# Optimization experiments

Measured on AMD Instinct MI355X. Metric: run time of the kernel, lower is better.

## Reference

```python
import jax, jax.numpy as jnp
import numpy as np

B, T, M, Q = 1024, 336, 1, 9
DFF, H, L = 7, 1024, 2
D_IN = DFF + M      # decoder input per step
D_OUT = M * Q       # quantile outputs per step


def setup_inputs() -> dict:
    key = jax.random.key(0)
    ks = jax.random.split(key, 16)
    s = 1.0 / np.sqrt(H)

    def rn(k, shape, scale):
        return (jax.random.normal(k, shape, jnp.float32) * scale).astype(jnp.float32)

    return {
        "batchsize": B,
        "Y_teacher": rn(ks[0], (B, T, M), 1.0),
        "inp_y": rn(ks[1], (B, 1, M), 1.0),
        "h": rn(ks[2], (L, B, H), 0.1),
        "c": rn(ks[3], (L, B, H), 0.1),
        "future_features": rn(ks[4], (B, T, DFF), 1.0),
        "horizon_span": T,
        "teacher_forcing": 0,
        "teacher_forcing_prob": 0,
        # LSTM layer 0 (input size D_IN) and layer 1 (input size H), PyTorch i,f,g,o gate order
        "W_ih0": rn(ks[5], (4 * H, D_IN), s),
        "W_hh0": rn(ks[6], (4 * H, H), s),
        "b_ih0": rn(ks[7], (4 * H,), s),
        "b_hh0": rn(ks[8], (4 * H,), s),
        "W_ih1": rn(ks[9], (4 * H, H), s),
        "W_hh1": rn(ks[10], (4 * H, H), s),
        "b_ih1": rn(ks[11], (4 * H,), s),
        "b_hh1": rn(ks[12], (4 * H,), s),
        # output projection d_hidden -> M*Q
        "W_out": rn(ks[13], (D_OUT, H), s),
        "b_out": rn(ks[14], (D_OUT,), s),
    }


def reference(batchsize, Y_teacher, inp_y, h, c, future_features, horizon_span,
              teacher_forcing, teacher_forcing_prob,
              W_ih0, W_hh0, b_ih0, b_hh0, W_ih1, W_hh1, b_ih1, b_hh1,
              W_out, b_out):
    m = inp_y.shape[-1]
    Wih = (W_ih0, W_ih1)
    Whh = (W_hh0, W_hh1)
    bih = (b_ih0, b_ih1)
    bhh = (b_hh0, b_hh1)

    def step(carry, f_t):
        hs, cs, y_prev = carry            # hs,cs: [L,B,H]; y_prev: [B,M]; f_t: [B,DFF]
        x = jnp.concatenate([y_prev, f_t], axis=-1)   # [B, D_IN]
        new_h, new_c = [], []
        for l in range(len(Wih)):
            gates = x @ Wih[l].T + bih[l] + hs[l] @ Whh[l].T + bhh[l]  # [B, 4H]
            i_, f_, g_, o_ = jnp.split(gates, 4, axis=-1)
            c_new = jax.nn.sigmoid(f_) * cs[l] + jax.nn.sigmoid(i_) * jnp.tanh(g_)
            h_new = jax.nn.sigmoid(o_) * jnp.tanh(c_new)
            new_h.append(h_new)
            new_c.append(c_new)
            x = h_new
        y = x @ W_out.T + b_out           # [B, M*Q]
        return (jnp.stack(new_h), jnp.stack(new_c), y[:, :m]), y

    ff = jnp.swapaxes(future_features, 0, 1)          # [T, B, DFF]
    _, ys = jax.lax.scan(step, (h, c, inp_y[:, 0, :]), ff)
    out = jnp.swapaxes(ys, 0, 1)                      # [B, T, M*Q]
    return out.reshape(batchsize, horizon_span, m, -1)
```

## Files before the change

### kernel.cpp

```cpp
#include <hip/hip_runtime.h>

typedef _Float16 f16;
typedef __attribute__((ext_vector_type(8))) _Float16 f16x8;
typedef __attribute__((ext_vector_type(4))) float f32x4;

#define NBATCH 1024
#define NH 1024
#define NT 336
#define NDFF 7
#define NQ 9
#define K0 1088
#define K1 2048
#define OUTSTRIDE (NT * NQ)

__device__ __forceinline__ float sigf(float x) { return 1.0f / (1.0f + __expf(-x)); }
__device__ __forceinline__ float tanhfast(float x) { return 1.0f - 2.0f / (__expf(2.0f * x) + 1.0f); }

__device__ __forceinline__ void gll16(const void* g, void* l) {
  __builtin_amdgcn_global_load_lds((const __attribute__((address_space(1))) void*)g,
                                   (__attribute__((address_space(3))) void*)l, 16, 0, 0);
}

__global__ void pack_w0(const float* __restrict__ Wih0, const float* __restrict__ Whh0,
                        f16* __restrict__ Wp0) {
  const int idx = blockIdx.x * 256 + threadIdx.x;
  if (idx >= 4096 * K0) return;
  const int j = idx / K0;
  const int dk = idx - j * K0;
  const int sk = (dk & ~63) | ((dk & 63) ^ ((j & 7) << 3));
  float v;
  if (sk < 8) v = Wih0[j * 8 + sk];
  else if (sk < 64) v = 0.0f;
  else v = Whh0[(size_t)j * NH + (sk - 64)];
  Wp0[idx] = (f16)v;
}

__global__ void pack_w1(const float* __restrict__ Wih1, const float* __restrict__ Whh1,
                        f16* __restrict__ Wp1) {
  const int idx = blockIdx.x * 256 + threadIdx.x;
  const int j = idx >> 11;
  const int dk = idx & 2047;
  const int sk = (dk & ~63) | ((dk & 63) ^ ((j & 7) << 3));
  const float v = (sk < 1024) ? Wih1[(size_t)j * NH + sk]
                              : Whh1[(size_t)j * NH + (sk - 1024)];
  Wp1[idx] = (f16)v;
}

__global__ void pack_bias(const float* __restrict__ a0, const float* __restrict__ b0,
                          const float* __restrict__ a1, const float* __restrict__ b1,
                          float* __restrict__ bias0, float* __restrict__ bias1) {
  const int j = blockIdx.x * 256 + threadIdx.x;
  if (j < 4096) { bias0[j] = a0[j] + b0[j]; bias1[j] = a1[j] + b1[j]; }
}

__global__ void init_state(const float* __restrict__ h_in, const float* __restrict__ c_in,
                           f16* __restrict__ h0, f16* __restrict__ h1,
                           float* __restrict__ c0, float* __restrict__ c1) {
  const int idx = blockIdx.x * 256 + threadIdx.x;
  const int l = idx >> 20;
  const int rc = idx & 1048575;
  const int row = rc >> 10;
  const int dk = idx & 1023;
  const int sk = (dk & ~63) | ((dk & 63) ^ ((row & 7) << 3));
  const float hv = h_in[((size_t)l << 20) + ((size_t)row << 10) + sk];
  if (l == 0) { h0[rc] = (f16)hv; c0[rc] = c_in[idx]; }
  else        { h1[rc] = (f16)hv; c1[rc] = c_in[idx]; }
}

__global__ void final_y(const float* __restrict__ ypartT, const float* __restrict__ bout,
                        float* __restrict__ dout) {
  const int idx = blockIdx.x * 256 + threadIdx.x;
  const int row = idx & 1023;
  const int q = idx >> 10;
  float s = bout[q];
#pragma unroll
  for (int nb2 = 0; nb2 < 32; ++nb2) s += ypartT[(((q << 5) + nb2) << 10) + row];
  dout[(size_t)row * OUTSTRIDE + 335 * NQ + q] = s;
}

template <int IS_S1>
__global__ __launch_bounds__(256, 1) void step_kernel(
    const f16* __restrict__ Wp, const float* __restrict__ bias,
    const f16* __restrict__ hA, const f16* __restrict__ hA2,
    float* __restrict__ cbuf, f16* __restrict__ hout,
    const float* __restrict__ ff, const float* __restrict__ inpy,
    float* __restrict__ ypartT, const float* __restrict__ Wout,
    const float* __restrict__ bout, float* __restrict__ dout, int t) {
  constexpr int NKT = IS_S1 ? (K1 / 64) : (K0 / 64);
  constexpr int LDSZ = IS_S1 ? (65536 + 128 * 33 * 4) : 65536;
  __shared__ __align__(16) unsigned char lds8[LDSZ];

  const int tid = threadIdx.x;
  const int wv = tid >> 6;
  const int ln = tid & 63;
  const int blk = blockIdx.x;
  const int rb = (blk >> 3) & 7;
  const int cb = (blk & 7) * 4 + (blk >> 6);
  const int row0 = rb * 128;
  const int hcol0 = cb * 32;

  auto stageB = [&](int kt, int buf) {
#pragma unroll
    for (int i = 0; i < 4; ++i) {
      const int ci = wv * 4 + i;
      const int tr = ci * 8 + (ln >> 3);
      const int j = ((tr >> 5) << 10) + hcol0 + (tr & 31);
      const f16* g = Wp + (size_t)j * (IS_S1 ? K1 : K0) + kt * 64 + (ln & 7) * 8;
      gll16(g, lds8 + buf * 32768 + 16384 + ci * 1024);
    }
  };
  auto stageA = [&](int kt, int buf) {
    const f16* src;
    int kb;
    if (IS_S1) {
      if (kt < 16) { src = hA; kb = kt * 64; }
      else { src = hA2; kb = (kt - 16) * 64; }
    } else { src = hA; kb = (kt - 1) * 64; }
#pragma unroll
    for (int i = 0; i < 4; ++i) {
      const int ci = wv * 4 + i;
      const int r = ci * 8 + (ln >> 3);
      const f16* g = src + (size_t)(row0 + r) * NH + kb + (ln & 7) * 8;
      gll16(g, lds8 + buf * 32768 + ci * 1024);
    }
  };

  if (!IS_S1) {
    if (tid < 128) {
      const int row = row0 + tid;
      float y0;
      if (t == 0) {
        y0 = inpy[row];
      } else {
        y0 = bout[0];
        const float* yp = ypartT + row;
#pragma unroll
        for (int nb2 = 0; nb2 < 32; ++nb2) y0 += yp[nb2 << 10];
      }
      const float* fsrc = ff + ((size_t)row * NT + t) * NDFF;
      f16x8 xv;
      xv[0] = (f16)y0;
#pragma unroll
      for (int jj = 0; jj < 7; ++jj) xv[1 + jj] = (f16)fsrc[jj];
      *(f16x8*)(lds8 + tid * 128 + ((tid & 7) << 4)) = xv;
    }
    f16x8 zv;
#pragma unroll
    for (int jj = 0; jj < 8; ++jj) zv[jj] = (f16)0.0f;
    for (int idx = tid; idx < 128 * 7; idx += 256) {
      const int r = idx / 7;
      const int ch = 1 + (idx - r * 7);
      *(f16x8*)(lds8 + r * 128 + ((ch ^ (r & 7)) << 4)) = zv;
    }
    if (t > 0 && cb < NQ && tid < 128) {
      const int q = cb;
      const int row = row0 + tid;
      float s = bout[q];
      const float* yp = ypartT + ((size_t)(q << 5) << 10) + row;
#pragma unroll
      for (int nb2 = 0; nb2 < 32; ++nb2) s += yp[nb2 << 10];
      dout[(size_t)row * OUTSTRIDE + (t - 1) * NQ + q] = s;
    }
    stageB(0, 0);
  } else {
    stageA(0, 0);
    stageB(0, 0);
  }
  __syncthreads();

  f32x4 acc[2][8];
  const f32x4 zf = {0.0f, 0.0f, 0.0f, 0.0f};
#pragma unroll
  for (int m = 0; m < 2; ++m)
#pragma unroll
    for (int n = 0; n < 8; ++n) acc[m][n] = zf;

  const int lanerow = ln & 15;
  const int xm = (ln & 7) << 4;
  const int kgrp = (ln >> 4) << 4;

  for (int kt = 0; kt < NKT; ++kt) {
    const int bcur = kt & 1;
    if (kt + 1 < NKT) { stageA(kt + 1, bcur ^ 1); stageB(kt + 1, bcur ^ 1); }
    const unsigned char* Ab = lds8 + bcur * 32768;
    const unsigned char* Bb = Ab + 16384;
#pragma unroll
    for (int ks = 0; ks < 2; ++ks) {
      const int kb = (kgrp + ks * 64) ^ xm;
      f16x8 afr[2], bfr[8];
#pragma unroll
      for (int m = 0; m < 2; ++m)
        afr[m] = *(const f16x8*)(Ab + (wv * 32 + m * 16 + lanerow) * 128 + kb);
#pragma unroll
      for (int n = 0; n < 8; ++n)
        bfr[n] = *(const f16x8*)(Bb + (n * 16 + lanerow) * 128 + kb);
#pragma unroll
      for (int m = 0; m < 2; ++m)
#pragma unroll
        for (int n = 0; n < 8; ++n)
          acc[m][n] = __builtin_amdgcn_mfma_f32_16x16x32_f16(afr[m], bfr[n], acc[m][n], 0, 0, 0);
    }
    __syncthreads();
  }

  float* hbuf = (float*)(lds8 + 65536);
#pragma unroll
  for (int m = 0; m < 2; ++m) {
#pragma unroll
    for (int hs = 0; hs < 2; ++hs) {
      const int hcol = hcol0 + hs * 16 + lanerow;
      const float bi = bias[hcol];
      const float bf = bias[NH + hcol];
      const float bg = bias[2 * NH + hcol];
      const float bo = bias[3 * NH + hcol];
      const f32x4 vi = acc[m][0 + hs];
      const f32x4 vf = acc[m][2 + hs];
      const f32x4 vg = acc[m][4 + hs];
      const f32x4 vo = acc[m][6 + hs];
#pragma unroll
      for (int r = 0; r < 4; ++r) {
        const int rloc = wv * 32 + m * 16 + ((ln >> 4) << 2) + r;
        const int row = row0 + rloc;
        const size_t cidx = (size_t)row * NH + hcol;
        const float c_old = cbuf[cidx];
        const float ig = sigf(vi[r] + bi);
        const float fg = sigf(vf[r] + bf);
        const float gg = tanhfast(vg[r] + bg);
        const float og = sigf(vo[r] + bo);
        const float cn = fg * c_old + ig * gg;
        const float hn = og * tanhfast(cn);
        cbuf[cidx] = cn;
        const int cc2 = (hcol & 63) << 1;
        *(f16*)((unsigned char*)hout + (size_t)row * 2048 + ((hcol >> 6) << 7) +
                (cc2 ^ ((row & 7) << 4))) = (f16)hn;
        if (IS_S1) hbuf[rloc * 33 + hs * 16 + lanerow] = hn;
      }
    }
  }
  if (IS_S1) {
    __syncthreads();
    for (int task = tid; task < 128 * NQ; task += 256) {
      const int rloc = task & 127;
      const int q = task >> 7;
      const float* wq = Wout + q * NH + hcol0;
      float s = 0.0f;
#pragma unroll
      for (int c2 = 0; c2 < 32; ++c2) s += hbuf[rloc * 33 + c2] * wq[c2];
      ypartT[(size_t)((q << 5) + cb) * 1024 + row0 + rloc] = s;
    }
  }
}

extern "C" void kernel_launch(void* const* d_in, const int* in_sizes, int n_in,
                              void* d_out, int out_size, void* d_ws, size_t ws_size,
                              hipStream_t stream) {
  const float* inpy = (const float*)d_in[2];
  const float* h_in = (const float*)d_in[3];
  const float* c_in = (const float*)d_in[4];
  const float* ff   = (const float*)d_in[5];
  const float* Wih0 = (const float*)d_in[9];
  const float* Whh0 = (const float*)d_in[10];
  const float* bih0 = (const float*)d_in[11];
  const float* bhh0 = (const float*)d_in[12];
  const float* Wih1 = (const float*)d_in[13];
  const float* Whh1 = (const float*)d_in[14];
  const float* bih1 = (const float*)d_in[15];
  const float* bhh1 = (const float*)d_in[16];
  const float* Wout = (const float*)d_in[17];
  const float* bout = (const float*)d_in[18];
  float* dout = (float*)d_out;

  unsigned char* ws = (unsigned char*)d_ws;
  size_t off = 0;
  auto alloc = [&](size_t bytes) -> void* {
    void* p = ws + off;
    off += (bytes + 255) & ~(size_t)255;
    return p;
  };
  f16* Wp0 = (f16*)alloc((size_t)4096 * K0 * 2);
  f16* Wp1 = (f16*)alloc((size_t)4096 * K1 * 2);
  f16* h0b0 = (f16*)alloc((size_t)NBATCH * NH * 2);
  f16* h0b1 = (f16*)alloc((size_t)NBATCH * NH * 2);
  f16* h1b0 = (f16*)alloc((size_t)NBATCH * NH * 2);
  f16* h1b1 = (f16*)alloc((size_t)NBATCH * NH * 2);
  float* c0 = (float*)alloc((size_t)NBATCH * NH * 4);
  float* c1 = (float*)alloc((size_t)NBATCH * NH * 4);
  float* bias0 = (float*)alloc(4096 * 4);
  float* bias1 = (float*)alloc(4096 * 4);
  float* ypartT = (float*)alloc((size_t)NQ * 32 * 1024 * 4);
  f16* h0b[2] = {h0b0, h0b1};
  f16* h1b[2] = {h1b0, h1b1};

  pack_w0<<<(4096 * K0) / 256, 256, 0, stream>>>(Wih0, Whh0, Wp0);
  pack_w1<<<(4096 * K1) / 256, 256, 0, stream>>>(Wih1, Whh1, Wp1);
  pack_bias<<<16, 256, 0, stream>>>(bih0, bhh0, bih1, bhh1, bias0, bias1);
  init_state<<<(2 * NBATCH * NH) / 256, 256, 0, stream>>>(h_in, c_in, h0b[0], h1b[0], c0, c1);

  for (int t = 0; t < NT; ++t) {
    const int p = t & 1;
    step_kernel<0><<<256, 256, 0, stream>>>(Wp0, bias0, h0b[p], nullptr, c0, h0b[1 - p],
                                            ff, inpy, ypartT, nullptr, bout, dout, t);
    step_kernel<1><<<256, 256, 0, stream>>>(Wp1, bias1, h0b[1 - p], h1b[p], c1, h1b[1 - p],
                                            nullptr, nullptr, ypartT, Wout, bout, dout, t);
  }
  final_y<<<36, 256, 0, stream>>>(ypartT, bout, dout);
}
```

Measured before the change: 17.67 ms.

## Triple-buffer LDS staging and reshape wave tiling with gate-interleaved weight packing

Moves the per-step LSTM GEMM from a double-buffered loop with two syncs per k-tile to a three-stage ring buffer, two tiles in flight, fine-grained vmcnt waits and one barrier per iteration. Weights are repacked so each column block's four gates sit contiguously, which lets waves use a 2x2 layout (64 rows x 64 cols each) instead of 4x1. The aim is to hide global-to-LDS latency and cut LDS fragment reads per MFMA. In exchange it needs 96KB of LDS and relies on hand-placed waitcnt and s_setprio.

```diff
diff --git a/kernel.cpp b/kernel.cpp
--- a/kernel.cpp
+++ b/kernel.cpp
@@ -24,10 +24,13 @@
 __global__ void pack_w0(const float* __restrict__ Wih0, const float* __restrict__ Whh0,
                         f16* __restrict__ Wp0) {
   const int idx = blockIdx.x * 256 + threadIdx.x;
-  if (idx >= 4096 * K0) return;
-  const int j = idx / K0;
-  const int dk = idx - j * K0;
-  const int sk = (dk & ~63) | ((dk & 63) ^ ((j & 7) << 3));
+  const int pr = idx / K0;
+  const int dk = idx - pr * K0;
+  const int cb = pr >> 7, p = pr & 127;
+  const int gate = (p >> 4) & 3;
+  const int hl = ((p >> 6) << 4) | (p & 15);
+  const int j = (gate << 10) + (cb << 5) + hl;
+  const int sk = (dk & ~63) | ((dk & 63) ^ ((p & 7) << 3));
   float v;
   if (sk < 8) v = Wih0[j * 8 + sk];
   else if (sk < 64) v = 0.0f;
@@ -38,9 +41,13 @@
 __global__ void pack_w1(const float* __restrict__ Wih1, const float* __restrict__ Whh1,
                         f16* __restrict__ Wp1) {
   const int idx = blockIdx.x * 256 + threadIdx.x;
-  const int j = idx >> 11;
+  const int pr = idx >> 11;
   const int dk = idx & 2047;
-  const int sk = (dk & ~63) | ((dk & 63) ^ ((j & 7) << 3));
+  const int cb = pr >> 7, p = pr & 127;
+  const int gate = (p >> 4) & 3;
+  const int hl = ((p >> 6) << 4) | (p & 15);
+  const int j = (gate << 10) + (cb << 5) + hl;
+  const int sk = (dk & ~63) | ((dk & 63) ^ ((p & 7) << 3));
   const float v = (sk < 1024) ? Wih1[(size_t)j * NH + sk]
                               : Whh1[(size_t)j * NH + (sk - 1024)];
   Wp1[idx] = (f16)v;
@@ -86,13 +93,15 @@
     const float* __restrict__ ff, const float* __restrict__ inpy,
     float* __restrict__ ypartT, const float* __restrict__ Wout,
     const float* __restrict__ bout, float* __restrict__ dout, int t) {
-  constexpr int NKT = IS_S1 ? (K1 / 64) : (K0 / 64);
-  constexpr int LDSZ = IS_S1 ? (65536 + 128 * 33 * 4) : 65536;
+  constexpr int KDIM = IS_S1 ? K1 : K0;
+  constexpr int NKT = KDIM / 64;
+  constexpr int LDSZ = IS_S1 ? (98304 + 128 * 33 * 4) : 98304;
   __shared__ __align__(16) unsigned char lds8[LDSZ];
 
   const int tid = threadIdx.x;
   const int wv = tid >> 6;
   const int ln = tid & 63;
+  const int wr = wv >> 1, wc = wv & 1;
   const int blk = blockIdx.x;
   const int rb = (blk >> 3) & 7;
   const int cb = (blk & 7) * 4 + (blk >> 6);
@@ -104,8 +113,7 @@
     for (int i = 0; i < 4; ++i) {
       const int ci = wv * 4 + i;
       const int tr = ci * 8 + (ln >> 3);
-      const int j = ((tr >> 5) << 10) + hcol0 + (tr & 31);
-      const f16* g = Wp + (size_t)j * (IS_S1 ? K1 : K0) + kt * 64 + (ln & 7) * 8;
+      const f16* g = Wp + (size_t)(cb * 128 + tr) * KDIM + kt * 64 + (ln & 7) * 8;
       gll16(g, lds8 + buf * 32768 + 16384 + ci * 1024);
     }
   };
@@ -162,79 +170,90 @@
       dout[(size_t)row * OUTSTRIDE + (t - 1) * NQ + q] = s;
     }
     stageB(0, 0);
+    stageA(1, 1); stageB(1, 1);
   } else {
-    stageA(0, 0);
-    stageB(0, 0);
-  }
-  __syncthreads();
-
-  f32x4 acc[2][8];
+    stageA(0, 0); stageB(0, 0);
+    stageA(1, 1); stageB(1, 1);
+  }
+  asm volatile("s_waitcnt lgkmcnt(0)" ::: "memory");
+
+  f32x4 acc[4][4];
   const f32x4 zf = {0.0f, 0.0f, 0.0f, 0.0f};
 #pragma unroll
-  for (int m = 0; m < 2; ++m)
-#pragma unroll
-    for (int n = 0; n < 8; ++n) acc[m][n] = zf;
+  for (int m = 0; m < 4; ++m)
+#pragma unroll
+    for (int n = 0; n < 4; ++n) acc[m][n] = zf;
 
   const int lanerow = ln & 15;
   const int xm = (ln & 7) << 4;
   const int kgrp = (ln >> 4) << 4;
+  int bc = 0;
 
   for (int kt = 0; kt < NKT; ++kt) {
-    const int bcur = kt & 1;
-    if (kt + 1 < NKT) { stageA(kt + 1, bcur ^ 1); stageB(kt + 1, bcur ^ 1); }
-    const unsigned char* Ab = lds8 + bcur * 32768;
+    __builtin_amdgcn_sched_barrier(0);
+    if (kt + 1 < NKT) {
+      asm volatile("s_waitcnt vmcnt(8)" ::: "memory");
+    } else {
+      asm volatile("s_waitcnt vmcnt(0)" ::: "memory");
+    }
+    __builtin_amdgcn_s_barrier();
+    __builtin_amdgcn_sched_barrier(0);
+    if (kt + 2 < NKT) {
+      const int nb = (bc == 0) ? 2 : bc - 1;
+      stageA(kt + 2, nb);
+      stageB(kt + 2, nb);
+    }
+    const unsigned char* Ab = lds8 + bc * 32768;
     const unsigned char* Bb = Ab + 16384;
 #pragma unroll
     for (int ks = 0; ks < 2; ++ks) {
       const int kb = (kgrp + ks * 64) ^ xm;
-      f16x8 afr[2], bfr[8];
-#pragma unroll
-      for (int m = 0; m < 2; ++m)
-        afr[m] = *(const f16x8*)(Ab + (wv * 32 + m * 16 + lanerow) * 128 + kb);
-#pragma unroll
-      for (int n = 0; n < 8; ++n)
-        bfr[n] = *(const f16x8*)(Bb + (n * 16 + lanerow) * 128 + kb);
-#pragma unroll
-      for (int m = 0; m < 2; ++m)
-#pragma unroll
-        for (int n = 0; n < 8; ++n)
+      f16x8 afr[4], bfr[4];
+#pragma unroll
+      for (int m = 0; m < 4; ++m)
+        afr[m] = *(const f16x8*)(Ab + (wr * 64 + m * 16 + lanerow) * 128 + kb);
+#pragma unroll
+      for (int n = 0; n < 4; ++n)
+        bfr[n] = *(const f16x8*)(Bb + (wc * 64 + n * 16 + lanerow) * 128 + kb);
+      __builtin_amdgcn_s_setprio(1);
+#pragma unroll
+      for (int m = 0; m < 4; ++m)
+#pragma unroll
+        for (int n = 0; n < 4; ++n)
           acc[m][n] = __builtin_amdgcn_mfma_f32_16x16x32_f16(afr[m], bfr[n], acc[m][n], 0, 0, 0);
-    }
-    __syncthreads();
-  }
-
-  float* hbuf = (float*)(lds8 + 65536);
-#pragma unroll
-  for (int m = 0; m < 2; ++m) {
-#pragma unroll
-    for (int hs = 0; hs < 2; ++hs) {
-      const int hcol = hcol0 + hs * 16 + lanerow;
-      const float bi = bias[hcol];
-      const float bf = bias[NH + hcol];
-      const float bg = bias[2 * NH + hcol];
-      const float bo = bias[3 * NH + hcol];
-      const f32x4 vi = acc[m][0 + hs];
-      const f32x4 vf = acc[m][2 + hs];
-      const f32x4 vg = acc[m][4 + hs];
-      const f32x4 vo = acc[m][6 + hs];
-#pragma unroll
-      for (int r = 0; r < 4; ++r) {
-        const int rloc = wv * 32 + m * 16 + ((ln >> 4) << 2) + r;
-        const int row = row0 + rloc;
-        const size_t cidx = (size_t)row * NH + hcol;
-        const float c_old = cbuf[cidx];
-        const float ig = sigf(vi[r] + bi);
-        const float fg = sigf(vf[r] + bf);
-        const float gg = tanhfast(vg[r] + bg);
-        const float og = sigf(vo[r] + bo);
-        const float cn = fg * c_old + ig * gg;
-        const float hn = og * tanhfast(cn);
-        cbuf[cidx] = cn;
-        const int cc2 = (hcol & 63) << 1;
-        *(f16*)((unsigned char*)hout + (size_t)row * 2048 + ((hcol >> 6) << 7) +
-                (cc2 ^ ((row & 7) << 4))) = (f16)hn;
-        if (IS_S1) hbuf[rloc * 33 + hs * 16 + lanerow] = hn;
-      }
+      __builtin_amdgcn_s_setprio(0);
+    }
+    bc = (bc == 2) ? 0 : bc + 1;
+  }
+
+  float* hbuf = (float*)(lds8 + 98304);
+  const int hcol = hcol0 + wc * 16 + lanerow;
+  const float bi = bias[hcol];
+  const float bff = bias[NH + hcol];
+  const float bg = bias[2 * NH + hcol];
+  const float bo = bias[3 * NH + hcol];
+#pragma unroll
+  for (int m = 0; m < 4; ++m) {
+    const f32x4 vi = acc[m][0];
+    const f32x4 vf = acc[m][1];
+    const f32x4 vg = acc[m][2];
+    const f32x4 vo = acc[m][3];
+#pragma unroll
+    for (int r = 0; r < 4; ++r) {
+      const int rloc = wr * 64 + m * 16 + ((ln >> 4) << 2) + r;
+      const int row = row0 + rloc;
+      const size_t cidx = (size_t)row * NH + hcol;
+      const float c_old = cbuf[cidx];
+      const float ig = sigf(vi[r] + bi);
+      const float fg = sigf(vf[r] + bff);
+      const float gg = tanhfast(vg[r] + bg);
+      const float og = sigf(vo[r] + bo);
+      const float cn = fg * c_old + ig * gg;
+      const float hn = og * tanhfast(cn);
+      cbuf[cidx] = cn;
+      *(f16*)((unsigned char*)hout + (size_t)row * 2048 + ((hcol >> 6) << 7) +
+              (((hcol & 63) << 1) ^ ((row & 7) << 4))) = (f16)hn;
+      if (IS_S1) hbuf[rloc * 33 + wc * 16 + lanerow] = hn;
     }
   }
   if (IS_S1) {
```

Measured after the change: 15.05 ms. 14.8% less time.
